# Kernel optimization log

Measured on AMD Instinct MI355X. Metric: run time of the kernel, lower is better.

The kernel has to match this reference:

```python
import jax, jax.numpy as jnp
import numpy as np

D = 64; H = 8; HD = 8; L = 3; FFN = 256
MAX_CHUNKS = 1024; MCL = 16


def rms_norm(x, w, eps=1e-6):
    return x * w * jax.lax.rsqrt(jnp.mean(x * x, axis=-1, keepdims=True) + eps)


def rope(x):
    # x: [B, S, H, HD]
    S, hd = x.shape[1], x.shape[-1]
    half = hd // 2
    freqs = 1.0 / (10000.0 ** (jnp.arange(half, dtype=x.dtype) * 2.0 / hd))
    ang = jnp.arange(S, dtype=x.dtype)[:, None] * freqs  # [S, half]
    cos = jnp.cos(ang)[None, :, None, :]
    sin = jnp.sin(ang)[None, :, None, :]
    x1, x2 = x[..., :half], x[..., half:]
    return jnp.concatenate([x1 * cos - x2 * sin, x1 * sin + x2 * cos], axis=-1)


def block(x, wq, wk, wv, wo, g1, g2, w1, w2):
    B, S, _ = x.shape
    h = rms_norm(x, g1)
    q = rope((h @ wq).reshape(B, S, H, HD))
    k = rope((h @ wk).reshape(B, S, H, HD))
    v = (h @ wv).reshape(B, S, H, HD)
    scores = jnp.einsum('bqhd,bkhd->bhqk', q, k) / jnp.sqrt(jnp.asarray(HD, x.dtype))
    causal = jnp.tril(jnp.ones((S, S), dtype=bool))
    scores = jnp.where(causal, scores, jnp.asarray(-1e30, x.dtype))
    attn = jax.nn.softmax(scores, axis=-1)
    o = jnp.einsum('bhqk,bkhd->bqhd', attn, v).reshape(B, S, D)
    x = x + o @ wo
    h2 = rms_norm(x, g2)
    return x + jax.nn.gelu(h2 @ w1, approximate=False) @ w2


def setup_inputs() -> dict:
    key = jax.random.key(0)
    ks = jax.random.split(key, 12)
    B, S = 4, 2048
    s = 1.0 / np.sqrt(D)
    return {
        'x': jax.random.normal(ks[0], (B, S, D), jnp.float32),
        'pad_token_vector': jax.random.normal(ks[1], (D,), jnp.float32),
        'x_ids': jax.random.randint(ks[2], (B, S), 0, 256),
        'pad_token_id': 257,
        'Wq': jax.random.normal(ks[3], (L, D, D), jnp.float32) * s,
        'Wk': jax.random.normal(ks[4], (L, D, D), jnp.float32) * s,
        'Wv': jax.random.normal(ks[5], (L, D, D), jnp.float32) * s,
        'Wo': jax.random.normal(ks[6], (L, D, D), jnp.float32) * s,
        'ln1': jnp.ones((L, D), jnp.float32),
        'ln2': jnp.ones((L, D), jnp.float32),
        'W1': jax.random.normal(ks[7], (L, D, FFN), jnp.float32) * s,
        'W2': jax.random.normal(ks[8], (L, FFN, D), jnp.float32) * (1.0 / np.sqrt(FFN)),
        'Whead': jax.random.normal(ks[9], (D, 2), jnp.float32) * s,
        'bhead': jnp.zeros((2,), jnp.float32),
    }


def reference(x, pad_token_vector, x_ids, pad_token_id, Wq, Wk, Wv, Wo, ln1, ln2, W1, W2, Whead, bhead):
    B, S, _ = x.shape
    h = x
    for l in range(L):
        h = block(h, Wq[l], Wk[l], Wv[l], Wo[l], ln1[l], ln2[l], W1[l], W2[l])
    logits = h @ Whead + bhead  # [B, S, 2]
    end_mask = logits[..., 0] > logits[..., 1]  # [B, S]
    t = jnp.arange(S)
    # fallback: if a row has no end, mark the last position as an end
    has_end = jnp.any(end_mask, axis=-1, keepdims=True)
    end_mask = jnp.where(has_end, end_mask, t[None, :] == S - 1)
    em = end_mask.astype(jnp.int32)
    num_ends = jnp.sum(em, axis=-1)                 # [B] = number of chunks
    chunk_id = jnp.cumsum(em, axis=-1) - em         # exclusive count of prior ends
    prev_end = jnp.concatenate([jnp.ones((B, 1), bool), end_mask[:, :-1]], axis=1)
    start_marker = jnp.where(prev_end, t[None, :], -1)
    start = jax.lax.associative_scan(jnp.maximum, start_marker, axis=-1)  # cummax -> chunk start per token
    pos = t[None, :] - start                        # position within chunk
    valid = (chunk_id < num_ends[:, None]) & (chunk_id < MAX_CHUNKS) & (pos < MCL)
    c_idx = jnp.where(valid, chunk_id, MAX_CHUNKS)  # invalid -> dummy chunk, sliced off
    p_idx = jnp.where(valid, pos, 0)
    b_idx = jnp.arange(B)[:, None]
    out = jnp.broadcast_to(pad_token_vector, (B, MAX_CHUNKS + 1, MCL, D))
    out = out.at[b_idx, c_idx, p_idx].set(h)[:, :MAX_CHUNKS]
    ids = jnp.full((B, MAX_CHUNKS + 1, MCL), pad_token_id, dtype=x_ids.dtype)
    ids = ids.at[b_idx, c_idx, p_idx].set(x_ids)[:, :MAX_CHUNKS]
    reg_term = jnp.mean(logits[..., 1])
    return out, ids, reg_term
```

## Files before the change

kernel.cpp:

```cpp
#include <hip/hip_runtime.h>
#include <math.h>

constexpr int D   = 64;
constexpr int H   = 8;
constexpr int HD  = 8;
constexpr int NL  = 3;
constexpr int FFNx= 256;
constexpr int Bb  = 4;
constexpr int Ss  = 2048;
constexpr int NT  = Bb * Ss;
constexpr int MAXC= 1024;
constexpr int MCL = 16;

constexpr int QW   = 128;
constexpr int CH   = 128;
constexpr int TPB  = 136;
constexpr int BPB  = 68;
constexpr int PBSZ = 1152;

constexpr size_t WX  = 0;
constexpr size_t WQ  = 524288;
constexpr size_t WKV = 2621440;
constexpr size_t WO  = 3670016;
constexpr size_t WPB = 4194304;
constexpr size_t WL1 = 9764864;
constexpr size_t WEM = WL1 + NT;
constexpr size_t WCP = WEM + NT;
constexpr size_t WCT = WCP + NT;
constexpr size_t WST = WCT + Ss*4;

constexpr float LOG2E = 1.4426950408889634f;

typedef float v2f  __attribute__((ext_vector_type(2)));
typedef float f16v __attribute__((ext_vector_type(16)));
using ckv_t = const __attribute__((address_space(4))) f16v*;

__device__ __forceinline__ float rdlane(float v, int l) {
    return __builtin_bit_cast(float, __builtin_amdgcn_readlane(__builtin_bit_cast(int, v), l));
}

__global__ void k_init(const float* __restrict__ x, float* __restrict__ X,
                       float* __restrict__ ct, float* __restrict__ st) {
    int i = blockIdx.x * blockDim.x + threadIdx.x;
    constexpr int N4 = NT * D / 4;
    if (i < N4) ((float4*)X)[i] = ((const float4*)x)[i];
    if (i < Ss * 4) {
        int s = i >> 2, f = i & 3;
        const float fr[4] = {1.0f, 0.1f, 0.01f, 0.001f};
        float ang = (float)s * fr[f];
        ct[i] = cosf(ang);
        st[i] = sinf(ang);
    }
}

__global__ __launch_bounds__(256) void k_qkv(
    const float* __restrict__ X, const float* __restrict__ Wq,
    const float* __restrict__ Wk, const float* __restrict__ Wv,
    const float* __restrict__ g1, const float* __restrict__ ct,
    const float* __restrict__ st, float* __restrict__ Q,
    float* __restrict__ KV) {
    __shared__ float wq_s[D*D], wk_s[D*D], wv_s[D*D];
    __shared__ float g_s[D];
    int tid = threadIdx.x;
    for (int i = tid; i < D*D; i += 256) {
        wq_s[i] = Wq[i]; wk_s[i] = Wk[i]; wv_s[i] = Wv[i];
    }
    if (tid < D) g_s[tid] = g1[tid];
    __syncthreads();
    int w = tid >> 6, d = tid & 63;
    int t0 = blockIdx.x * 16;
    for (int it = 0; it < 4; ++it) {
        int t = t0 + it*4 + w;
        float xv = X[t*D + d];
        float ss = xv * xv;
        #pragma unroll
        for (int off = 32; off; off >>= 1) ss += __shfl_xor(ss, off);
        float r = 1.0f / sqrtf(ss * (1.0f/D) + 1e-6f);
        float h = xv * g_s[d] * r;
        float aq = 0.f, ak = 0.f, av = 0.f;
        #pragma unroll
        for (int j = 0; j < D; ++j) {
            float hj = rdlane(h, j);
            aq += hj * wq_s[j*D + d];
            ak += hj * wk_s[j*D + d];
            av += hj * wv_s[j*D + d];
        }
        int s  = t & (Ss - 1);
        int e  = d & 7;
        int fi = e & 3;
        float c  = ct[s*4 + fi];
        float sn = st[s*4 + fi];
        float pq = __shfl_xor(aq, 4);
        float pk = __shfl_xor(ak, 4);
        float rq, rk;
        if (e < 4) { rq = aq*c - pq*sn; rk = ak*c - pk*sn; }
        else       { rq = pq*sn + aq*c; rk = pk*sn + ak*c; }
        Q[t*D + d] = rq;
        int bq = t >> 11;
        int hh = d >> 3;
        float* kvp = KV + ((((size_t)(bq*H + hh))*Ss + s) << 4);
        kvp[e]     = rk;
        kvp[8 + e] = av;
    }
}

template<bool DIAG>
__device__ __forceinline__ void attn_loop(
    ckv_t kvs, int L, int rel0,
    const v2f* __restrict__ q01, v2f& l01, v2f* __restrict__ oP) {
    #pragma unroll 4
    for (int j = 0; j < 64; ++j) {
        f16v kv = kvs[j];
        v2f acc;
        acc  = q01[0] * (v2f){kv[0], kv[0]};
        acc += q01[1] * (v2f){kv[1], kv[1]};
        acc += q01[2] * (v2f){kv[2], kv[2]};
        acc += q01[3] * (v2f){kv[3], kv[3]};
        acc += q01[4] * (v2f){kv[4], kv[4]};
        acc += q01[5] * (v2f){kv[5], kv[5]};
        acc += q01[6] * (v2f){kv[6], kv[6]};
        acc += q01[7] * (v2f){kv[7], kv[7]};
        if (DIAG) {
            int rel = rel0 + j;
            if (rel > L)      acc.x = -1e30f;
            if (rel > L + 64) acc.y = -1e30f;
        }
        v2f p;
        p.x = __builtin_amdgcn_exp2f(acc.x);
        p.y = __builtin_amdgcn_exp2f(acc.y);
        l01 += p;
        oP[0] += p * (v2f){kv[8],  kv[8]};
        oP[1] += p * (v2f){kv[9],  kv[9]};
        oP[2] += p * (v2f){kv[10], kv[10]};
        oP[3] += p * (v2f){kv[11], kv[11]};
        oP[4] += p * (v2f){kv[12], kv[12]};
        oP[5] += p * (v2f){kv[13], kv[13]};
        oP[6] += p * (v2f){kv[14], kv[14]};
        oP[7] += p * (v2f){kv[15], kv[15]};
    }
}

__global__ __launch_bounds__(256) void k_attn2(
    const float* __restrict__ Qg, const float* __restrict__ KV,
    float* __restrict__ PB) {
    __shared__ float comb[2][PBSZ];
    int xcd  = blockIdx.x & 7;
    int slot = blockIdx.x >> 3;
    int bhg  = slot / BPB;
    int blk  = slot - bhg * BPB;
    int bh   = bhg * 8 + xcd;
    int wvu  = __builtin_amdgcn_readfirstlane(threadIdx.x >> 6);
    int pair = wvu >> 1;
    int half = wvu & 1;
    int widb = blk * 2 + pair;
    int L = threadIdx.x & 63;
    int rem = widb;
    int s = 0;
    while (rem >= 16 - s) { rem -= 16 - s; ++s; }
    int t = s + rem;
    int b = bh >> 3, h = bh & 7;
    int qmin = t * QW;
    int k0 = s * CH + half * 64;

    const float SC = 0.35355339059327373f * LOG2E;
    const float* qp = Qg + ((size_t)(b*Ss + qmin + L))*D + h*HD;
    float4 qa0 = *(const float4*)(qp);
    float4 qb0 = *(const float4*)(qp + 4);
    float4 qa1 = *(const float4*)(qp + 64*D);
    float4 qb1 = *(const float4*)(qp + 64*D + 4);
    v2f q01[8];
    q01[0] = (v2f){qa0.x*SC, qa1.x*SC};
    q01[1] = (v2f){qa0.y*SC, qa1.y*SC};
    q01[2] = (v2f){qa0.z*SC, qa1.z*SC};
    q01[3] = (v2f){qa0.w*SC, qa1.w*SC};
    q01[4] = (v2f){qb0.x*SC, qb1.x*SC};
    q01[5] = (v2f){qb0.y*SC, qb1.y*SC};
    q01[6] = (v2f){qb0.z*SC, qb1.z*SC};
    q01[7] = (v2f){qb0.w*SC, qb1.w*SC};

    v2f l01 = (v2f){0.f, 0.f};
    v2f oP[8];
    #pragma unroll
    for (int e = 0; e < 8; ++e) oP[e] = (v2f){0.f, 0.f};

    ckv_t kvs = (ckv_t)(unsigned long long)(KV + (((size_t)bh*Ss + k0) << 4));
    if (s == t) attn_loop<true >(kvs, L, half*64, q01, l01, oP);
    else        attn_loop<false>(kvs, L, half*64, q01, l01, oP);

    if (half == 1) {
        comb[pair][L]      = l01.x;
        comb[pair][64 + L] = l01.y;
        #pragma unroll
        for (int e = 0; e < 8; ++e) {
            comb[pair][128 + e*128 + L]      = oP[e].x;
            comb[pair][128 + e*128 + 64 + L] = oP[e].y;
        }
    }
    __syncthreads();
    if (half == 0) {
        float* pb = PB + ((size_t)bh * TPB + widb) * PBSZ;
        pb[L]      = l01.x + comb[pair][L];
        pb[64 + L] = l01.y + comb[pair][64 + L];
        #pragma unroll
        for (int e = 0; e < 8; ++e) {
            pb[128 + e*128 + L]      = oP[e].x + comb[pair][128 + e*128 + L];
            pb[128 + e*128 + 64 + L] = oP[e].y + comb[pair][128 + e*128 + 64 + L];
        }
    }
}

__global__ __launch_bounds__(128) void k_comb(const float* __restrict__ PB,
                                              float* __restrict__ Og) {
    int qs = threadIdx.x;
    int t  = blockIdx.x & 15;
    int bh = blockIdx.x >> 4;
    int b = bh >> 3, h = bh & 7;
    float Lx = 0.f;
    float O[8] = {0,0,0,0,0,0,0,0};
    for (int s3 = 0; s3 <= t; ++s3) {
        int idx = 16*s3 - (s3*(s3-1))/2 + (t - s3);
        const float* pb = PB + (size_t)(bh*TPB + idx) * PBSZ;
        Lx += pb[qs];
        #pragma unroll
        for (int e = 0; e < 8; ++e) O[e] += pb[128 + e*128 + qs];
    }
    float inv = 1.0f / Lx;
    float* op = Og + ((size_t)(b*Ss + t*QW + qs))*D + h*HD;
    #pragma unroll
    for (int e = 0; e < 8; ++e) op[e] = O[e] * inv;
}

__global__ __launch_bounds__(256) void k_post1(
    float* __restrict__ X, const float* __restrict__ Og,
    const float* __restrict__ Wo) {
    __shared__ float ws_[D*D];
    int tid = threadIdx.x;
    for (int i = tid; i < D*D; i += 256) ws_[i] = Wo[i];
    __syncthreads();
    int w = tid >> 6, d = tid & 63;
    int t0 = blockIdx.x * 32;
    for (int it = 0; it < 8; ++it) {
        int t = t0 + it*4 + w;
        float ov = Og[t*D + d];
        float a = 0.f;
        #pragma unroll
        for (int j = 0; j < D; ++j) a += rdlane(ov, j) * ws_[j*D + d];
        X[t*D + d] += a;
    }
}

__global__ __launch_bounds__(256) void k_ffn(
    float* __restrict__ X, const float* __restrict__ g2,
    const float* __restrict__ W1, const float* __restrict__ W2) {
    __shared__ __align__(16) float h2t[64][20];
    __shared__ float part[16][16];
    __shared__ float g_s[D];
    __shared__ __align__(16) float ult[FFNx][20];
    __shared__ float red[4][16][D];
    int tid = threadIdx.x;
    if (tid < D) g_s[tid] = g2[tid];
    int t0 = blockIdx.x * 16;
    int tk = tid >> 4, li = tid & 15;
    float x0 = X[(t0+tk)*D + li];
    float x1 = X[(t0+tk)*D + li + 16];
    float x2 = X[(t0+tk)*D + li + 32];
    float x3 = X[(t0+tk)*D + li + 48];
    part[tk][li] = x0*x0 + x1*x1 + x2*x2 + x3*x3;
    __syncthreads();
    if (tid < 16) {
        float s = 0.f;
        #pragma unroll
        for (int i = 0; i < 16; ++i) s += part[tid][i];
        part[tid][0] = 1.0f / sqrtf(s * (1.0f/D) + 1e-6f);
    }
    __syncthreads();
    float r = part[tk][0];
    h2t[li][tk]      = x0 * g_s[li]      * r;
    h2t[li + 16][tk] = x1 * g_s[li + 16] * r;
    h2t[li + 32][tk] = x2 * g_s[li + 32] * r;
    h2t[li + 48][tk] = x3 * g_s[li + 48] * r;
    __syncthreads();
    {
        int f = tid;
        v2f acc2[8];
        #pragma unroll
        for (int i = 0; i < 8; ++i) acc2[i] = (v2f){0.f, 0.f};
        for (int j = 0; j < D; ++j) {
            float wv = W1[j*FFNx + f];
            v2f wv2 = (v2f){wv, wv};
            const float4* hp = (const float4*)&h2t[j][0];
            float4 a0 = hp[0], a1 = hp[1], a2 = hp[2], a3 = hp[3];
            const v2f* a0v = (const v2f*)&a0;
            const v2f* a1v = (const v2f*)&a1;
            const v2f* a2v = (const v2f*)&a2;
            const v2f* a3v = (const v2f*)&a3;
            acc2[0] += a0v[0]*wv2;  acc2[1] += a0v[1]*wv2;
            acc2[2] += a1v[0]*wv2;  acc2[3] += a1v[1]*wv2;
            acc2[4] += a2v[0]*wv2;  acc2[5] += a2v[1]*wv2;
            acc2[6] += a3v[0]*wv2;  acc2[7] += a3v[1]*wv2;
        }
        #pragma unroll
        for (int i = 0; i < 8; ++i) {
            float ua = acc2[i].x;
            float ub = acc2[i].y;
            ua = 0.5f * ua * (1.0f + erff(ua * 0.70710678118654752f));
            ub = 0.5f * ub * (1.0f + erff(ub * 0.70710678118654752f));
            ult[f][2*i]     = ua;
            ult[f][2*i + 1] = ub;
        }
    }
    __syncthreads();
    {
        int d = tid & 63, fp = tid >> 6;
        v2f acc2[8];
        #pragma unroll
        for (int i = 0; i < 8; ++i) acc2[i] = (v2f){0.f, 0.f};
        for (int fo = 0; fo < 64; ++fo) {
            int f = fp*64 + fo;
            float wv = W2[f*D + d];
            v2f wv2 = (v2f){wv, wv};
            const float4* up = (const float4*)&ult[f][0];
            float4 u0 = up[0], u1 = up[1], u2 = up[2], u3 = up[3];
            const v2f* u0v = (const v2f*)&u0;
            const v2f* u1v = (const v2f*)&u1;
            const v2f* u2v = (const v2f*)&u2;
            const v2f* u3v = (const v2f*)&u3;
            acc2[0] += u0v[0]*wv2;  acc2[1] += u0v[1]*wv2;
            acc2[2] += u1v[0]*wv2;  acc2[3] += u1v[1]*wv2;
            acc2[4] += u2v[0]*wv2;  acc2[5] += u2v[1]*wv2;
            acc2[6] += u3v[0]*wv2;  acc2[7] += u3v[1]*wv2;
        }
        #pragma unroll
        for (int i = 0; i < 8; ++i) {
            red[fp][2*i][d]     = acc2[i].x;
            red[fp][2*i + 1][d] = acc2[i].y;
        }
        __syncthreads();
        int tk2 = tid >> 6;
        #pragma unroll
        for (int k = 0; k < 4; ++k) {
            int tt = tk2 + k*4;
            float sum = red[0][tt][d] + red[1][tt][d] + red[2][tt][d] + red[3][tt][d];
            X[(t0 + tt)*D + d] += sum;
        }
    }
}

__global__ __launch_bounds__(256) void k_head(
    const float* __restrict__ X, const float* __restrict__ Wh,
    const float* __restrict__ bh, float* __restrict__ logit1,
    int* __restrict__ em) {
    int tid = threadIdx.x;
    int w = tid >> 6, d = tid & 63;
    int t = blockIdx.x*4 + w;
    float xv = X[t*D + d];
    float p0 = xv * Wh[d*2];
    float p1 = xv * Wh[d*2 + 1];
    #pragma unroll
    for (int off = 32; off; off >>= 1) {
        p0 += __shfl_xor(p0, off);
        p1 += __shfl_xor(p1, off);
    }
    if (d == 0) {
        float l0 = p0 + bh[0], l1 = p1 + bh[1];
        em[t] = (l0 > l1) ? 1 : 0;
        logit1[t] = l1;
    }
}

__global__ void k_reg(const float* __restrict__ logit1, float* __restrict__ outreg) {
    __shared__ float red[256];
    int tid = threadIdx.x;
    float s = 0.f;
    for (int i = tid; i < NT; i += 256) s += logit1[i];
    red[tid] = s;
    __syncthreads();
    for (int off = 128; off; off >>= 1) {
        if (tid < off) red[tid] += red[tid + off];
        __syncthreads();
    }
    if (tid == 0) *outreg = red[0] * (1.0f / NT);
}

__global__ __launch_bounds__(256) void k_scan(const int* __restrict__ em,
                                              int* __restrict__ cp) {
    __shared__ int ssum[256], smax[256];
    __shared__ int sany, stot;
    int b = blockIdx.x, tid = threadIdx.x;
    const int* e = em + b*Ss;
    int base = tid * 8;
    int loc[8];
    int lsum = 0, lor = 0;
    #pragma unroll
    for (int i = 0; i < 8; ++i) { loc[i] = e[base + i]; lsum += loc[i]; lor |= loc[i]; }
    ssum[tid] = lor;
    __syncthreads();
    if (tid == 0) { int a = 0; for (int i = 0; i < 256; ++i) a |= ssum[i]; sany = a; }
    __syncthreads();
    int any = sany;
    __syncthreads();
    if (!any && tid == 255) { loc[7] = 1; lsum = 1; }
    int prev = (tid == 0) ? 1 : e[base - 1];
    if (!any && tid) prev = 0;
    int mk[8];
    int lmax = -1;
    #pragma unroll
    for (int i = 0; i < 8; ++i) {
        int pe = (i == 0) ? prev : loc[i - 1];
        if (i == 7 && !any && tid == 255) pe = e[base + 6];
        mk[i] = pe ? (base + i) : -1;
        lmax = max(lmax, mk[i]);
    }
    ssum[tid] = lsum; smax[tid] = lmax;
    __syncthreads();
    if (tid == 0) {
        int rs = 0, rm = -1;
        for (int i = 0; i < 256; ++i) {
            int ts = ssum[i], tm = smax[i];
            ssum[i] = rs; smax[i] = rm;
            rs += ts; rm = max(rm, tm);
        }
        stot = rs;
    }
    __syncthreads();
    int run = ssum[tid], rmax = smax[tid], tot = stot;
    int* cpb = cp + b*Ss;
    #pragma unroll
    for (int i = 0; i < 8; ++i) {
        int s = base + i;
        rmax = max(rmax, mk[i]);
        int chunk = run;
        run += loc[i];
        int pos = s - rmax;
        bool valid = (chunk < tot) && (chunk < MAXC) && (pos < MCL);
        cpb[s] = valid ? (chunk * MCL + pos) : -1;
    }
}

__global__ void k_fill(float* __restrict__ out, const float* __restrict__ pad,
                       const int* __restrict__ padid) {
    int i = blockIdx.x * blockDim.x + threadIdx.x;
    constexpr int N4  = Bb * MAXC * MCL * D / 4;
    constexpr int NI4 = Bb * MAXC * MCL / 4;
    if (i < N4) {
        ((float4*)out)[i] = ((const float4*)pad)[i & 15];
    } else if (i < N4 + NI4) {
        float pv = (float)(*padid);
        float4 v; v.x = pv; v.y = pv; v.z = pv; v.w = pv;
        ((float4*)out)[i] = v;
    }
}

__global__ __launch_bounds__(256) void k_scatter(
    const float* __restrict__ X, const int* __restrict__ cp,
    const int* __restrict__ ids, float* __restrict__ out) {
    int tid = threadIdx.x;
    int w = tid >> 6, d = tid & 63;
    int t = blockIdx.x*4 + w;
    int c = cp[t];
    if (c < 0) return;
    int b = t >> 11;
    float* dst = out + ((size_t)(b * MAXC * MCL) + c) * D;
    dst[d] = X[t*D + d];
    if (d == 0)
        out[(size_t)Bb*MAXC*MCL*D + (size_t)b*MAXC*MCL + c] = (float)ids[t];
}

extern "C" void kernel_launch(void* const* d_in, const int* in_sizes, int n_in,
                              void* d_out, int out_size, void* d_ws, size_t ws_size,
                              hipStream_t stream) {
    const float* x    = (const float*)d_in[0];
    const float* pad  = (const float*)d_in[1];
    const int*   xids = (const int*)  d_in[2];
    const int*   padid= (const int*)  d_in[3];
    const float* Wq   = (const float*)d_in[4];
    const float* Wk   = (const float*)d_in[5];
    const float* Wv   = (const float*)d_in[6];
    const float* Wo   = (const float*)d_in[7];
    const float* ln1  = (const float*)d_in[8];
    const float* ln2  = (const float*)d_in[9];
    const float* W1   = (const float*)d_in[10];
    const float* W2   = (const float*)d_in[11];
    const float* Wh   = (const float*)d_in[12];
    const float* bh   = (const float*)d_in[13];
    float* out = (float*)d_out;
    float* ws  = (float*)d_ws;

    float* X  = ws + WX;
    float* Qb = ws + WQ;
    float* KVb= ws + WKV;
    float* Ob = ws + WO;
    float* PBb= ws + WPB;
    float* L1b= ws + WL1;
    int*   EMb= (int*)(ws + WEM);
    int*   CPb= (int*)(ws + WCP);
    float* ct = ws + WCT;
    float* st = ws + WST;

    k_init<<<2048, 256, 0, stream>>>(x, X, ct, st);
    for (int l = 0; l < NL; ++l) {
        k_qkv <<<512, 256, 0, stream>>>(X, Wq + l*D*D, Wk + l*D*D, Wv + l*D*D,
                                        ln1 + l*D, ct, st, Qb, KVb);
        k_attn2<<<32*BPB, 256, 0, stream>>>(Qb, KVb, PBb);
        k_comb <<<32*16, 128, 0, stream>>>(PBb, Ob);
        k_post1<<<256, 256, 0, stream>>>(X, Ob, Wo + l*D*D);
        k_ffn  <<<NT/16, 256, 0, stream>>>(X, ln2 + l*D, W1 + l*D*FFNx, W2 + l*FFNx*D);
    }
    k_head<<<NT/4, 256, 0, stream>>>(X, Wh, bh, L1b, EMb);
    k_reg <<<1, 256, 0, stream>>>(L1b, out + (size_t)Bb*MAXC*MCL*D + Bb*MAXC*MCL);
    k_scan<<<Bb, 256, 0, stream>>>(EMb, CPb);
    k_fill<<<(Bb*MAXC*MCL*D/4 + Bb*MAXC*MCL/4 + 255)/256, 256, 0, stream>>>(out, pad, padid);
    k_scatter<<<NT/4, 256, 0, stream>>>(X, CPb, xids, out);
}
```

Baseline: 287.2 us.

## Fuse attention combine with output projection, head into FFN, and fill with scatter

Merges the partial-attention combine kernel with the Wo projection and residual add, so the intermediate attention output buffer is no longer written and re-read. The classification head moves into the last layer's FFN epilogue. The scan now builds an inverse slot-to-token map, so one output kernel writes each output slot once, either from X or the pad vector, replacing the fill-then-scatter pair. This cuts kernel launches and global memory traffic. In exchange, the combine grid is smaller (256 blocks) and each block stages Wo in shared memory, and the single-block-per-batch scan must now also initialise a 16K-entry map.

Result: no change. 282.0 us (-1.8%).

```diff
diff --git a/kernel.cpp b/kernel.cpp
--- a/kernel.cpp
+++ b/kernel.cpp
@@ -21,12 +21,11 @@
 constexpr size_t WX  = 0;
 constexpr size_t WQ  = 524288;
 constexpr size_t WKV = 2621440;
-constexpr size_t WO  = 3670016;
 constexpr size_t WPB = 4194304;
 constexpr size_t WL1 = 9764864;
 constexpr size_t WEM = WL1 + NT;
-constexpr size_t WCP = WEM + NT;
-constexpr size_t WCT = WCP + NT;
+constexpr size_t WINV= WEM + NT;
+constexpr size_t WCT = WINV + Bb*MAXC*MCL;
 constexpr size_t WST = WCT + Ss*4;
 
 constexpr float LOG2E = 1.4426950408889634f;
@@ -209,12 +208,21 @@
     }
 }
 
-__global__ __launch_bounds__(128) void k_comb(const float* __restrict__ PB,
-                                              float* __restrict__ Og) {
-    int qs = threadIdx.x;
-    int t  = blockIdx.x & 15;
-    int bh = blockIdx.x >> 4;
-    int b = bh >> 3, h = bh & 7;
+__global__ __launch_bounds__(256) void k_combo(
+    const float* __restrict__ PB, float* __restrict__ X,
+    const float* __restrict__ Wo) {
+    __shared__ float wo_s[D*D];
+    __shared__ float oT[32][65];
+    int tid = threadIdx.x;
+    int seg = blockIdx.x & 3;
+    int t   = (blockIdx.x >> 2) & 15;
+    int b   = blockIdx.x >> 6;
+    for (int i = tid; i < D*D; i += 256) wo_s[i] = Wo[i];
+
+    int h  = tid >> 5;
+    int ql = tid & 31;
+    int qs = seg*32 + ql;
+    int bh = b*8 + h;
     float Lx = 0.f;
     float O[8] = {0,0,0,0,0,0,0,0};
     for (int s3 = 0; s3 <= t; ++s3) {
@@ -225,33 +233,27 @@
         for (int e = 0; e < 8; ++e) O[e] += pb[128 + e*128 + qs];
     }
     float inv = 1.0f / Lx;
-    float* op = Og + ((size_t)(b*Ss + t*QW + qs))*D + h*HD;
     #pragma unroll
-    for (int e = 0; e < 8; ++e) op[e] = O[e] * inv;
-}
-
-__global__ __launch_bounds__(256) void k_post1(
-    float* __restrict__ X, const float* __restrict__ Og,
-    const float* __restrict__ Wo) {
-    __shared__ float ws_[D*D];
-    int tid = threadIdx.x;
-    for (int i = tid; i < D*D; i += 256) ws_[i] = Wo[i];
-    __syncthreads();
-    int w = tid >> 6, d = tid & 63;
-    int t0 = blockIdx.x * 32;
-    for (int it = 0; it < 8; ++it) {
-        int t = t0 + it*4 + w;
-        float ov = Og[t*D + d];
+    for (int e = 0; e < 8; ++e) oT[ql][h*8 + e] = O[e] * inv;
+    __syncthreads();
+
+    int d = tid & 63, wv = tid >> 6;
+    #pragma unroll 2
+    for (int k = 0; k < 8; ++k) {
+        int tt = wv*8 + k;
         float a = 0.f;
         #pragma unroll
-        for (int j = 0; j < D; ++j) a += rdlane(ov, j) * ws_[j*D + d];
-        X[t*D + d] += a;
-    }
-}
-
+        for (int j = 0; j < D; ++j) a += oT[tt][j] * wo_s[j*D + d];
+        X[((size_t)(b*Ss) + t*128 + seg*32 + tt)*D + d] += a;
+    }
+}
+
+template<bool HEAD>
 __global__ __launch_bounds__(256) void k_ffn(
     float* __restrict__ X, const float* __restrict__ g2,
-    const float* __restrict__ W1, const float* __restrict__ W2) {
+    const float* __restrict__ W1, const float* __restrict__ W2,
+    const float* __restrict__ Wh, const float* __restrict__ bhp,
+    float* __restrict__ logit1, int* __restrict__ em) {
     __shared__ __align__(16) float h2t[64][20];
     __shared__ float part[16][16];
     __shared__ float g_s[D];
@@ -341,30 +343,23 @@
         for (int k = 0; k < 4; ++k) {
             int tt = tk2 + k*4;
             float sum = red[0][tt][d] + red[1][tt][d] + red[2][tt][d] + red[3][tt][d];
-            X[(t0 + tt)*D + d] += sum;
-        }
-    }
-}
-
-__global__ __launch_bounds__(256) void k_head(
-    const float* __restrict__ X, const float* __restrict__ Wh,
-    const float* __restrict__ bh, float* __restrict__ logit1,
-    int* __restrict__ em) {
-    int tid = threadIdx.x;
-    int w = tid >> 6, d = tid & 63;
-    int t = blockIdx.x*4 + w;
-    float xv = X[t*D + d];
-    float p0 = xv * Wh[d*2];
-    float p1 = xv * Wh[d*2 + 1];
-    #pragma unroll
-    for (int off = 32; off; off >>= 1) {
-        p0 += __shfl_xor(p0, off);
-        p1 += __shfl_xor(p1, off);
-    }
-    if (d == 0) {
-        float l0 = p0 + bh[0], l1 = p1 + bh[1];
-        em[t] = (l0 > l1) ? 1 : 0;
-        logit1[t] = l1;
+            float xf = X[(t0 + tt)*D + d] + sum;
+            X[(t0 + tt)*D + d] = xf;
+            if (HEAD) {
+                float p0 = xf * Wh[d*2];
+                float p1 = xf * Wh[d*2 + 1];
+                #pragma unroll
+                for (int off = 32; off; off >>= 1) {
+                    p0 += __shfl_xor(p0, off);
+                    p1 += __shfl_xor(p1, off);
+                }
+                if (d == 0) {
+                    float l0 = p0 + bhp[0], l1 = p1 + bhp[1];
+                    em[t0 + tt] = (l0 > l1) ? 1 : 0;
+                    logit1[t0 + tt] = l1;
+                }
+            }
+        }
     }
 }
 
@@ -383,10 +378,13 @@
 }
 
 __global__ __launch_bounds__(256) void k_scan(const int* __restrict__ em,
-                                              int* __restrict__ cp) {
+                                              int* __restrict__ inv) {
     __shared__ int ssum[256], smax[256];
     __shared__ int sany, stot;
     int b = blockIdx.x, tid = threadIdx.x;
+    int* invb = inv + b * (MAXC*MCL);
+    for (int i = tid; i < MAXC*MCL; i += 256) invb[i] = -1;
+    __syncthreads();
     const int* e = em + b*Ss;
     int base = tid * 8;
     int loc[8];
@@ -424,7 +422,6 @@
     }
     __syncthreads();
     int run = ssum[tid], rmax = smax[tid], tot = stot;
-    int* cpb = cp + b*Ss;
     #pragma unroll
     for (int i = 0; i < 8; ++i) {
         int s = base + i;
@@ -433,37 +430,36 @@
         run += loc[i];
         int pos = s - rmax;
         bool valid = (chunk < tot) && (chunk < MAXC) && (pos < MCL);
-        cpb[s] = valid ? (chunk * MCL + pos) : -1;
-    }
-}
-
-__global__ void k_fill(float* __restrict__ out, const float* __restrict__ pad,
-                       const int* __restrict__ padid) {
+        if (valid) invb[chunk * MCL + pos] = b*Ss + s;
+    }
+}
+
+__global__ __launch_bounds__(256) void k_out(
+    const float* __restrict__ X, const float* __restrict__ pad,
+    const int* __restrict__ xids, const int* __restrict__ padid,
+    const int* __restrict__ inv, float* __restrict__ out) {
     int i = blockIdx.x * blockDim.x + threadIdx.x;
-    constexpr int N4  = Bb * MAXC * MCL * D / 4;
+    constexpr int NV4 = Bb * MAXC * MCL * D / 4;
     constexpr int NI4 = Bb * MAXC * MCL / 4;
-    if (i < N4) {
-        ((float4*)out)[i] = ((const float4*)pad)[i & 15];
-    } else if (i < N4 + NI4) {
+    if (i < NV4) {
+        int slot = i >> 4;
+        int d4 = i & 15;
+        int t = inv[slot];
+        float4 v = (t >= 0) ? ((const float4*)X)[t*16 + d4]
+                            : ((const float4*)pad)[d4];
+        ((float4*)out)[i] = v;
+    } else if (i < NV4 + NI4) {
+        int j = i - NV4;
         float pv = (float)(*padid);
-        float4 v; v.x = pv; v.y = pv; v.z = pv; v.w = pv;
+        int base = j * 4;
+        int t0_ = inv[base], t1_ = inv[base+1], t2_ = inv[base+2], t3_ = inv[base+3];
+        float4 v;
+        v.x = (t0_ >= 0) ? (float)xids[t0_] : pv;
+        v.y = (t1_ >= 0) ? (float)xids[t1_] : pv;
+        v.z = (t2_ >= 0) ? (float)xids[t2_] : pv;
+        v.w = (t3_ >= 0) ? (float)xids[t3_] : pv;
         ((float4*)out)[i] = v;
     }
-}
-
-__global__ __launch_bounds__(256) void k_scatter(
-    const float* __restrict__ X, const int* __restrict__ cp,
-    const int* __restrict__ ids, float* __restrict__ out) {
-    int tid = threadIdx.x;
-    int w = tid >> 6, d = tid & 63;
-    int t = blockIdx.x*4 + w;
-    int c = cp[t];
-    if (c < 0) return;
-    int b = t >> 11;
-    float* dst = out + ((size_t)(b * MAXC * MCL) + c) * D;
-    dst[d] = X[t*D + d];
-    if (d == 0)
-        out[(size_t)Bb*MAXC*MCL*D + (size_t)b*MAXC*MCL + c] = (float)ids[t];
 }
 
 extern "C" void kernel_launch(void* const* d_in, const int* in_sizes, int n_in,
@@ -489,11 +485,10 @@
     float* X  = ws + WX;
     float* Qb = ws + WQ;
     float* KVb= ws + WKV;
-    float* Ob = ws + WO;
     float* PBb= ws + WPB;
     float* L1b= ws + WL1;
     int*   EMb= (int*)(ws + WEM);
-    int*   CPb= (int*)(ws + WCP);
+    int*   INVb=(int*)(ws + WINV);
     float* ct = ws + WCT;
     float* st = ws + WST;
 
@@ -502,13 +497,17 @@
         k_qkv <<<512, 256, 0, stream>>>(X, Wq + l*D*D, Wk + l*D*D, Wv + l*D*D,
                                         ln1 + l*D, ct, st, Qb, KVb);
         k_attn2<<<32*BPB, 256, 0, stream>>>(Qb, KVb, PBb);
-        k_comb <<<32*16, 128, 0, stream>>>(PBb, Ob);
-        k_post1<<<256, 256, 0, stream>>>(X, Ob, Wo + l*D*D);
-        k_ffn  <<<NT/16, 256, 0, stream>>>(X, ln2 + l*D, W1 + l*D*FFNx, W2 + l*FFNx*D);
-    }
-    k_head<<<NT/4, 256, 0, stream>>>(X, Wh, bh, L1b, EMb);
+        k_combo<<<256, 256, 0, stream>>>(PBb, X, Wo + l*D*D);
+        if (l == NL - 1)
+            k_ffn<true ><<<NT/16, 256, 0, stream>>>(X, ln2 + l*D, W1 + l*D*FFNx,
+                                                    W2 + l*FFNx*D, Wh, bh, L1b, EMb);
+        else
+            k_ffn<false><<<NT/16, 256, 0, stream>>>(X, ln2 + l*D, W1 + l*D*FFNx,
+                                                    W2 + l*FFNx*D, nullptr, nullptr,
+                                                    nullptr, nullptr);
+    }
     k_reg <<<1, 256, 0, stream>>>(L1b, out + (size_t)Bb*MAXC*MCL*D + Bb*MAXC*MCL);
-    k_scan<<<Bb, 256, 0, stream>>>(EMb, CPb);
-    k_fill<<<(Bb*MAXC*MCL*D/4 + Bb*MAXC*MCL/4 + 255)/256, 256, 0, stream>>>(out, pad, padid);
-    k_scatter<<<NT/4, 256, 0, stream>>>(X, CPb, xids, out);
-}
+    k_scan<<<Bb, 256, 0, stream>>>(EMb, INVb);
+    k_out <<<(Bb*MAXC*MCL*D/4 + Bb*MAXC*MCL/4 + 255)/256, 256, 0, stream>>>(
+        X, pad, xids, padid, INVb, out);
+}
```
